# Kernel tuning notes

Measured on AMD Instinct MI355X. Metric: run time of the kernel, lower is better.

## Reference

```python
import jax, jax.numpy as jnp
import numpy as np

EOS = 1e-10
N = 6000          # nnodes
E = 192000        # n_edges (avg degree 32)
D_IN = 512        # input_dim
H = 128           # hidden_dim
ALPHA = 1.0
TEMP = 1.0
BIAS = 1e-4


def setup_inputs() -> dict:
    key = jax.random.key(0)
    k1, k2, k3, k4, k5, k6, k7 = jax.random.split(key, 7)
    features = jax.random.normal(k1, (N, D_IN), dtype=jnp.float32)
    edges = jax.random.randint(k2, (2, E), 0, N)
    # params: embedding Linear(D_IN->H) and edge MLP Linear(2H->1)
    w_emb = jax.random.normal(k3, (D_IN, H), dtype=jnp.float32) * 0.05
    b_emb = jnp.zeros((H,), jnp.float32)
    w_mlp = jax.random.normal(k4, (2 * H, 1), dtype=jnp.float32) * 0.05
    b_mlp = jnp.zeros((1,), jnp.float32)
    # gumbel-sigmoid noise: eps = (bias-(1-bias))*u + (1-bias)  in [bias, 1-bias]
    u = jax.random.uniform(k5, (E,), dtype=jnp.float32)
    eps = (BIAS - (1.0 - BIAS)) * u + (1.0 - BIAS)
    gate_noise = jnp.log(eps) - jnp.log(1.0 - eps)
    return {"features": features, "edges": edges, "w_emb": w_emb, "b_emb": b_emb,
            "w_mlp": w_mlp, "b_mlp": b_mlp, "gate_noise": gate_noise}


def _normalize_sym(adj):
    d = adj.sum(axis=1)
    inv = 1.0 / (jnp.sqrt(d) + EOS)
    return adj * inv[:, None] * inv[None, :]


def reference(features, edges, w_emb, b_emb, w_mlp, b_mlp, gate_noise):
    # node embeddings: single Linear + ReLU
    emb = jax.nn.relu(features @ w_emb + b_emb)              # [N, H]
    h0 = emb[edges[0]]                                       # [E, H]
    h1 = emb[edges[1]]                                       # [E, H]
    s1 = (jnp.concatenate([h0, h1], axis=1) @ w_mlp + b_mlp).ravel()
    s2 = (jnp.concatenate([h1, h0], axis=1) @ w_mlp + b_mlp).ravel()
    raw = (s1 + s2) * 0.5                                    # [E]
    # gumbel-sigmoid gating
    weights_lp = jax.nn.sigmoid((gate_noise + raw) / TEMP)
    weights_hp = 1.0 - weights_lp

    eye = jnp.eye(N, dtype=features.dtype)

    def build_adj(w):
        adj = jnp.zeros((N, N), features.dtype).at[edges[0], edges[1]].set(w)
        return _normalize_sym(adj + eye)

    adj_lp = build_adj(weights_lp)
    adj_hp = build_adj(weights_hp)
    mask = jnp.zeros((N, N), features.dtype).at[edges[0], edges[1]].set(1.0)
    adj_hp = eye - adj_hp * mask * ALPHA
    adj_unnorm = jnp.zeros((N, N), features.dtype).at[edges[0], edges[1]].set(1.0)
    return (adj_lp, adj_hp, weights_lp, weights_hp, adj_unnorm)
```

## Files before the change

### kernel.cpp

```cpp
#include <hip/hip_runtime.h>
#include <math.h>

#define NNODES 6000
#define NEDGES 192000
#define DIN 512
#define HDIM 128
#define ALPHA 1.0f
#define EOS 1e-10f
#define KMAX 256
#define CHUNK 1000

typedef float f32x4 __attribute__((ext_vector_type(4)));

static const size_t NN = (size_t)NNODES * (size_t)NNODES;

__global__ __launch_bounds__(128) void embed_g_kernel(
    const float* __restrict__ feat, const float* __restrict__ w_emb,
    const float* __restrict__ b_emb, const float* __restrict__ w_mlp,
    float* __restrict__ g, int* __restrict__ cnt) {
  __shared__ float sf[8 * DIN];
  __shared__ float red[2][8];
  const int t = threadIdx.x;
  const int nb = blockIdx.x * 8;

  if (t < 8) cnt[nb + t] = 0;

  const float4* f4 = (const float4*)(feat + (size_t)nb * DIN);
  float4* s4 = (float4*)sf;
#pragma unroll
  for (int k = 0; k < 8; ++k) s4[k * 128 + t] = f4[k * 128 + t];
  __syncthreads();

  const int h = t;
  float acc[8];
  const float b = b_emb[h];
#pragma unroll
  for (int n = 0; n < 8; ++n) acc[n] = b;

  const float4* sf4 = (const float4*)sf;
#pragma unroll 2
  for (int d4 = 0; d4 < DIN / 4; ++d4) {
    const float w0 = w_emb[(d4 * 4 + 0) * HDIM + h];
    const float w1 = w_emb[(d4 * 4 + 1) * HDIM + h];
    const float w2 = w_emb[(d4 * 4 + 2) * HDIM + h];
    const float w3 = w_emb[(d4 * 4 + 3) * HDIM + h];
#pragma unroll
    for (int n = 0; n < 8; ++n) {
      const float4 f = sf4[n * (DIN / 4) + d4];
      acc[n] += f.x * w0;
      acc[n] += f.y * w1;
      acc[n] += f.z * w2;
      acc[n] += f.w * w3;
    }
  }

  const float wv = 0.5f * (w_mlp[h] + w_mlp[HDIM + h]);
  const int lane = t & 63, wave = t >> 6;
#pragma unroll
  for (int n = 0; n < 8; ++n) {
    float v = fmaxf(acc[n], 0.0f) * wv;
    for (int off = 32; off > 0; off >>= 1) v += __shfl_down(v, off, 64);
    if (lane == 0) red[wave][n] = v;
  }
  __syncthreads();
  if (t < 8) g[nb + t] = red[0][t] + red[1][t];
}

__global__ __launch_bounds__(256) void edge_bucket_kernel(
    const int* __restrict__ edges, const float* __restrict__ g,
    const float* __restrict__ noise, const float* __restrict__ b_mlp,
    float* __restrict__ w_lp, float* __restrict__ w_hp,
    int* __restrict__ cnt, int* __restrict__ slots) {
  const int e = blockIdx.x * blockDim.x + threadIdx.x;
  if (e >= NEDGES) return;
  const int u = edges[e];
  const int v = edges[NEDGES + e];
  const float raw = g[u] + g[v] + b_mlp[0];
  const float x = noise[e] + raw;
  const float wl = 1.0f / (1.0f + __expf(-x));
  w_lp[e] = wl;
  w_hp[e] = 1.0f - wl;
  const int k = atomicAdd(&cnt[u], 1);
  if (k < KMAX) slots[(size_t)u * NNODES + k] = e;
}

__global__ __launch_bounds__(256) void row_dedup_deg_kernel(
    const int* __restrict__ edges, const float* __restrict__ w_lp,
    const float* __restrict__ w_hp, const int* __restrict__ cnt,
    int* __restrict__ slots, float* __restrict__ inv_lp,
    float* __restrict__ inv_hp) {
  __shared__ int se[4][KMAX];
  __shared__ int sv[4][KMAX];
  __shared__ float sl[4][KMAX];
  __shared__ float sh[4][KMAX];
  const int wid = threadIdx.x >> 6;
  const int lane = threadIdx.x & 63;
  const int r = blockIdx.x * 4 + wid;

  int k = cnt[r];
  if (k > KMAX) k = KMAX;
  int* srow = slots + (size_t)r * NNODES;
  for (int i = lane; i < k; i += 64) {
    const int e = srow[i];
    se[wid][i] = e;
    sv[wid][i] = edges[NEDGES + e];
    sl[wid][i] = w_lp[e];
    sh[wid][i] = w_hp[e];
  }
  __syncthreads();

  float suml = 0.0f, sumh = 0.0f;
  for (int i = lane; i < k; i += 64) {
    const int e = se[wid][i];
    const int v = sv[wid][i];
    int win = 1;
    for (int j = 0; j < k; ++j) {
      if (sv[wid][j] == v && se[wid][j] > e) { win = 0; break; }
    }
    if (win) {
      suml += sl[wid][i];
      sumh += sh[wid][i];
    }
    srow[i] = (e << 14) | (v << 1) | win;
  }
  for (int off = 32; off > 0; off >>= 1) {
    suml += __shfl_down(suml, off, 64);
    sumh += __shfl_down(sumh, off, 64);
  }
  if (lane == 0) {
    inv_lp[r] = 1.0f / (sqrtf(suml + 1.0f) + EOS);
    inv_hp[r] = 1.0f / (sqrtf(sumh + 1.0f) + EOS);
  }
}

__global__ __launch_bounds__(256) void paint_kernel(
    const float* __restrict__ w_lp, const float* __restrict__ w_hp,
    const float* __restrict__ inv_lp, const float* __restrict__ inv_hp,
    const int* __restrict__ cnt, float* __restrict__ adj_lp,
    float* __restrict__ adj_hp, float* __restrict__ unnorm) {
  __shared__ __align__(16) float chl[CHUNK];
  __shared__ __align__(16) float chh[CHUNK];
  __shared__ __align__(16) float chu[CHUNK];
  __shared__ int colw[KMAX + 1];
  __shared__ float vlp[KMAX + 1];
  __shared__ float vhp[KMAX + 1];
  __shared__ int colu[KMAX];
  __shared__ int skk, shas;

  const int t = threadIdx.x;
  const int r = blockIdx.x;
  int k = cnt[r];
  if (k > KMAX) k = KMAX;
  const float il = inv_lp[r];
  const float ih = inv_hp[r];

  float* lp_row = adj_lp + (size_t)r * NNODES;
  float* hp_row = adj_hp + (size_t)r * NNODES;
  float* un_row = unnorm + (size_t)r * NNODES;
  const int* srow = (const int*)un_row;

  if (t == 0) shas = 0;
  __syncthreads();

  if (t < k) {
    const int raw = srow[t];
    const int win = raw & 1;
    const int v = (raw >> 1) & 0x1FFF;
    const int e = (int)(((unsigned)raw) >> 14);
    const float wl = w_lp[e];
    const float wh = w_hp[e];
    colu[t] = v;
    if (v == r) shas = 1;
    if (win) {
      if (v == r) {
        colw[t] = r;
        vlp[t] = (wl + 1.0f) * il * il;
        vhp[t] = 1.0f - (wh + 1.0f) * ih * ih * ALPHA;
      } else {
        colw[t] = v;
        vlp[t] = wl * il * inv_lp[v];
        vhp[t] = -ALPHA * wh * ih * inv_hp[v];
      }
    } else {
      colw[t] = -1;
    }
  }
  __syncthreads();

  if (t == 0) {
    if (!shas) {
      colw[k] = r;
      vlp[k] = il * il;
      vhp[k] = 1.0f;
      skk = k + 1;
    } else {
      skk = k;
    }
  }
  __syncthreads();
  const int kk = skk;

  const f32x4 z = {0.0f, 0.0f, 0.0f, 0.0f};
  f32x4* chl4 = (f32x4*)chl;
  f32x4* chh4 = (f32x4*)chh;
  f32x4* chu4 = (f32x4*)chu;

  for (int c0 = 0; c0 < NNODES; c0 += CHUNK) {
    if (t < CHUNK / 4) {
      chl4[t] = z;
      chh4[t] = z;
      chu4[t] = z;
    }
    __syncthreads();
    for (int j = t; j < kk; j += 256) {
      const int d = colw[j] - c0;
      if ((unsigned)d < (unsigned)CHUNK) {
        chl[d] = vlp[j];
        chh[d] = vhp[j];
      }
    }
    for (int j = t; j < k; j += 256) {
      const int d = colu[j] - c0;
      if ((unsigned)d < (unsigned)CHUNK) chu[d] = 1.0f;
    }
    __syncthreads();
    if (t < CHUNK / 4) {
      const f32x4 L = chl4[t];
      const f32x4 H = chh4[t];
      const f32x4 U = chu4[t];
      __builtin_nontemporal_store(L, (f32x4*)(lp_row + c0) + t);
      __builtin_nontemporal_store(H, (f32x4*)(hp_row + c0) + t);
      __builtin_nontemporal_store(U, (f32x4*)(un_row + c0) + t);
    }
    __syncthreads();
  }
}

extern "C" void kernel_launch(void* const* d_in, const int* in_sizes, int n_in,
                              void* d_out, int out_size, void* d_ws,
                              size_t ws_size, hipStream_t stream) {
  const float* feat  = (const float*)d_in[0];
  const int*   edges = (const int*)d_in[1];
  const float* w_emb = (const float*)d_in[2];
  const float* b_emb = (const float*)d_in[3];
  const float* w_mlp = (const float*)d_in[4];
  const float* b_mlp = (const float*)d_in[5];
  const float* noise = (const float*)d_in[6];

  float* out    = (float*)d_out;
  float* adj_lp = out;
  float* adj_hp = out + NN;
  float* w_lp   = out + 2 * NN;
  float* w_hp   = w_lp + NEDGES;
  float* unnorm = w_hp + NEDGES;

  float* g      = (float*)d_ws;
  float* inv_lp = g + NNODES;
  float* inv_hp = inv_lp + NNODES;
  int*   cnt    = (int*)(inv_hp + NNODES);

  embed_g_kernel<<<NNODES / 8, 128, 0, stream>>>(feat, w_emb, b_emb, w_mlp, g,
                                                 cnt);

  edge_bucket_kernel<<<NEDGES / 256, 256, 0, stream>>>(
      edges, g, noise, b_mlp, w_lp, w_hp, cnt, (int*)unnorm);

  row_dedup_deg_kernel<<<NNODES / 4, 256, 0, stream>>>(
      edges, w_lp, w_hp, cnt, (int*)unnorm, inv_lp, inv_hp);

  paint_kernel<<<NNODES, 256, 0, stream>>>(w_lp, w_hp, inv_lp, inv_hp, cnt,
                                           adj_lp, adj_hp, unnorm);
}
```

Measured before the change: 530.3 us.

## Split paint kernel per output matrix with full-row LDS image and compact slots

Moves the per-row edge slot lists out of the unnorm output into a compact workspace buffer of KMAX ints per row. The paint kernel now launches one block per (matrix, row) pair instead of one per row. Each block builds the whole 6000-float row image in LDS and streams it out with nontemporal stores, replacing the chunked loop and its per-chunk barriers. This triples the block count and makes each block write only one matrix. The cost is about 24KB of LDS per block, which may limit occupancy, and each edge list is now reread once per matrix.

```diff
diff --git a/kernel.cpp b/kernel.cpp
--- a/kernel.cpp
+++ b/kernel.cpp
@@ -8,7 +8,6 @@
 #define ALPHA 1.0f
 #define EOS 1e-10f
 #define KMAX 256
-#define CHUNK 1000
 
 typedef float f32x4 __attribute__((ext_vector_type(4)));
 
@@ -81,7 +80,7 @@
   w_lp[e] = wl;
   w_hp[e] = 1.0f - wl;
   const int k = atomicAdd(&cnt[u], 1);
-  if (k < KMAX) slots[(size_t)u * NNODES + k] = e;
+  if (k < KMAX) slots[u * KMAX + k] = e;
 }
 
 __global__ __launch_bounds__(256) void row_dedup_deg_kernel(
@@ -99,7 +98,7 @@
 
   int k = cnt[r];
   if (k > KMAX) k = KMAX;
-  int* srow = slots + (size_t)r * NNODES;
+  int* srow = slots + r * KMAX;
   for (int i = lane; i < k; i += 64) {
     const int e = srow[i];
     se[wid][i] = e;
@@ -136,104 +135,88 @@
 __global__ __launch_bounds__(256) void paint_kernel(
     const float* __restrict__ w_lp, const float* __restrict__ w_hp,
     const float* __restrict__ inv_lp, const float* __restrict__ inv_hp,
-    const int* __restrict__ cnt, float* __restrict__ adj_lp,
-    float* __restrict__ adj_hp, float* __restrict__ unnorm) {
-  __shared__ __align__(16) float chl[CHUNK];
-  __shared__ __align__(16) float chh[CHUNK];
-  __shared__ __align__(16) float chu[CHUNK];
-  __shared__ int colw[KMAX + 1];
-  __shared__ float vlp[KMAX + 1];
-  __shared__ float vhp[KMAX + 1];
-  __shared__ int colu[KMAX];
+    const int* __restrict__ cnt, const int* __restrict__ slots,
+    float* __restrict__ adj_lp, float* __restrict__ adj_hp,
+    float* __restrict__ unnorm) {
+  __shared__ __align__(16) float img[NNODES];
+  __shared__ int col[KMAX + 1];
+  __shared__ float val[KMAX + 1];
   __shared__ int skk, shas;
+  __shared__ float sdiag;
 
   const int t = threadIdx.x;
-  const int r = blockIdx.x;
+  const int b = blockIdx.x;
+  const int m = b / NNODES;
+  const int r = b - m * NNODES;
+
   int k = cnt[r];
   if (k > KMAX) k = KMAX;
+
+  if (t == 0) {
+    shas = 0;
+    sdiag = 0.0f;
+  }
+  __syncthreads();
+
+  const int* srow = slots + r * KMAX;
   const float il = inv_lp[r];
   const float ih = inv_hp[r];
 
-  float* lp_row = adj_lp + (size_t)r * NNODES;
-  float* hp_row = adj_hp + (size_t)r * NNODES;
-  float* un_row = unnorm + (size_t)r * NNODES;
-  const int* srow = (const int*)un_row;
-
-  if (t == 0) shas = 0;
-  __syncthreads();
+  f32x4* img4 = (f32x4*)img;
+  const f32x4 z = {0.0f, 0.0f, 0.0f, 0.0f};
+  for (int i = t; i < NNODES / 4; i += 256) img4[i] = z;
 
   if (t < k) {
     const int raw = srow[t];
     const int win = raw & 1;
     const int v = (raw >> 1) & 0x1FFF;
     const int e = (int)(((unsigned)raw) >> 14);
-    const float wl = w_lp[e];
-    const float wh = w_hp[e];
-    colu[t] = v;
-    if (v == r) shas = 1;
-    if (win) {
+    if (m == 2) {
+      col[t] = v;
+      val[t] = 1.0f;
+    } else {
+      const float w = (m == 0) ? w_lp[e] : w_hp[e];
       if (v == r) {
-        colw[t] = r;
-        vlp[t] = (wl + 1.0f) * il * il;
-        vhp[t] = 1.0f - (wh + 1.0f) * ih * ih * ALPHA;
+        shas = 1;
+        if (win) sdiag = w;
+        col[t] = -1;
+      } else if (win) {
+        col[t] = v;
+        val[t] = (m == 0) ? w * il * inv_lp[v]
+                          : -ALPHA * w * ih * inv_hp[v];
       } else {
-        colw[t] = v;
-        vlp[t] = wl * il * inv_lp[v];
-        vhp[t] = -ALPHA * wh * ih * inv_hp[v];
+        col[t] = -1;
       }
-    } else {
-      colw[t] = -1;
     }
   }
   __syncthreads();
 
   if (t == 0) {
-    if (!shas) {
-      colw[k] = r;
-      vlp[k] = il * il;
-      vhp[k] = 1.0f;
+    if (m == 0) {
+      col[k] = r;
+      val[k] = (sdiag + 1.0f) * il * il;
+      skk = k + 1;
+    } else if (m == 1) {
+      col[k] = r;
+      val[k] = shas ? (1.0f - (sdiag + 1.0f) * ih * ih * ALPHA) : 1.0f;
       skk = k + 1;
     } else {
       skk = k;
     }
   }
   __syncthreads();
+
   const int kk = skk;
-
-  const f32x4 z = {0.0f, 0.0f, 0.0f, 0.0f};
-  f32x4* chl4 = (f32x4*)chl;
-  f32x4* chh4 = (f32x4*)chh;
-  f32x4* chu4 = (f32x4*)chu;
-
-  for (int c0 = 0; c0 < NNODES; c0 += CHUNK) {
-    if (t < CHUNK / 4) {
-      chl4[t] = z;
-      chh4[t] = z;
-      chu4[t] = z;
-    }
-    __syncthreads();
-    for (int j = t; j < kk; j += 256) {
-      const int d = colw[j] - c0;
-      if ((unsigned)d < (unsigned)CHUNK) {
-        chl[d] = vlp[j];
-        chh[d] = vhp[j];
-      }
-    }
-    for (int j = t; j < k; j += 256) {
-      const int d = colu[j] - c0;
-      if ((unsigned)d < (unsigned)CHUNK) chu[d] = 1.0f;
-    }
-    __syncthreads();
-    if (t < CHUNK / 4) {
-      const f32x4 L = chl4[t];
-      const f32x4 H = chh4[t];
-      const f32x4 U = chu4[t];
-      __builtin_nontemporal_store(L, (f32x4*)(lp_row + c0) + t);
-      __builtin_nontemporal_store(H, (f32x4*)(hp_row + c0) + t);
-      __builtin_nontemporal_store(U, (f32x4*)(un_row + c0) + t);
-    }
-    __syncthreads();
-  }
+  for (int j = t; j < kk; j += 256) {
+    const int c = col[j];
+    if (c >= 0) img[c] = val[j];
+  }
+  __syncthreads();
+
+  float* dst = (m == 0 ? adj_lp : (m == 1 ? adj_hp : unnorm)) +
+               (size_t)r * NNODES;
+  for (int i = t; i < NNODES / 4; i += 256)
+    __builtin_nontemporal_store(img4[i], (f32x4*)dst + i);
 }
 
 extern "C" void kernel_launch(void* const* d_in, const int* in_sizes, int n_in,
@@ -258,16 +241,18 @@
   float* inv_lp = g + NNODES;
   float* inv_hp = inv_lp + NNODES;
   int*   cnt    = (int*)(inv_hp + NNODES);
+  int*   slots  = cnt + NNODES;
 
   embed_g_kernel<<<NNODES / 8, 128, 0, stream>>>(feat, w_emb, b_emb, w_mlp, g,
                                                  cnt);
 
   edge_bucket_kernel<<<NEDGES / 256, 256, 0, stream>>>(
-      edges, g, noise, b_mlp, w_lp, w_hp, cnt, (int*)unnorm);
+      edges, g, noise, b_mlp, w_lp, w_hp, cnt, slots);
 
   row_dedup_deg_kernel<<<NNODES / 4, 256, 0, stream>>>(
-      edges, w_lp, w_hp, cnt, (int*)unnorm, inv_lp, inv_hp);
-
-  paint_kernel<<<NNODES, 256, 0, stream>>>(w_lp, w_hp, inv_lp, inv_hp, cnt,
-                                           adj_lp, adj_hp, unnorm);
-}
+      edges, w_lp, w_hp, cnt, slots, inv_lp, inv_hp);
+
+  paint_kernel<<<3 * NNODES, 256, 0, stream>>>(w_lp, w_hp, inv_lp, inv_hp,
+                                               cnt, slots, adj_lp, adj_hp,
+                                               unnorm);
+}
```

Result: faster. 514.3 us, median of 2 (-3.0%).
